# Optimization experiments

Hardware: AMD Instinct MI355X
Metric: run time of the kernel (lower is better)

The kernel has to match this reference:

```python
import jax, jax.numpy as jnp
import numpy as np
from jax import lax

B, C, H, W = 8, 128, 96, 96
EXPAN = 4           # expan_att_chans
NUM_CHANS = 2
NUM_HEADS = NUM_CHANS * EXPAN          # 8
HEAD_DIM = C * EXPAN // NUM_HEADS      # 64
EPS = 1e-12  # F.normalize eps


def _gconv(x, w, b, groups):
    # torch Conv2d(kernel=3, padding=1, groups=groups), OIHW weight layout
    y = lax.conv_general_dilated(x, w, (1, 1), 'SAME',
                                 feature_group_count=groups,
                                 dimension_numbers=('NCHW', 'OIHW', 'NCHW'))
    return y + b[None, :, None, None]


def setup_inputs() -> dict:
    key = jax.random.key(0)
    k0, k1, k2 = jax.random.split(key, 3)
    x = jax.random.normal(k0, (B, C, H, W), jnp.float32)
    w_qkv = jax.random.normal(k1, (C * EXPAN * 3, 1, 3, 3), jnp.float32) * 0.05
    b_qkv = jnp.zeros((C * EXPAN * 3,), jnp.float32)
    t = jnp.ones((1, NUM_HEADS, 1, 1), jnp.float32)
    w_fus = jax.random.normal(k2, (C, EXPAN, 3, 3), jnp.float32) * 0.05
    b_fus = jnp.zeros((C,), jnp.float32)
    return {"x": x, "w_qkv": w_qkv, "b_qkv": b_qkv, "t": t,
            "w_fus": w_fus, "b_fus": b_fus}


def reference(x, w_qkv, b_qkv, t, w_fus, b_fus):
    # depthwise-grouped qkv conv: [B, C*EXPAN*3, H, W]
    qkv = _gconv(x, w_qkv, b_qkv, C)
    # view(B, C, 3e, H, W).transpose(1,2) -> [B, 3e, C, H, W]
    qkv = qkv.reshape(B, C, 3 * EXPAN, H, W).transpose(0, 2, 1, 3, 4)
    q, k, v = jnp.split(qkv, 3, axis=1)  # each [B, EXPAN, C, H, W]

    def heads(a):
        return a.reshape(B, NUM_HEADS, HEAD_DIM, H * W)

    q, k, v = heads(q), heads(k), heads(v)

    def l2n(a):
        return a / jnp.maximum(jnp.linalg.norm(a, axis=-1, keepdims=True), EPS)

    q, k = l2n(q), l2n(k)
    attn = jnp.einsum('bhdn,bhen->bhde', q, k) * t   # [B, nh, hd, hd]
    attn = jax.nn.softmax(attn, axis=-1)
    o = jnp.einsum('bhde,bhen->bhdn', attn, v)       # [B, nh, hd, HW]
    # view(B, EXPAN, C, H, W).transpose(1,2).flatten(1,2) -> [B, C*EXPAN, H, W]
    o = o.reshape(B, EXPAN, C, H, W).transpose(0, 2, 1, 3, 4).reshape(B, C * EXPAN, H, W)
    return _gconv(o, w_fus, b_fus, C)
```

## Files before the change

kernel.cpp:

```cpp
#include <hip/hip_runtime.h>
#include <hip/hip_bf16.h>
#include <stdint.h>

#define BB     8
#define CC     128
#define HW     9216
#define NHEAD  8
#define HD     64
#define NCH    16
#define CHUNK  576

typedef __hip_bfloat16 bf16;
using frag16 = __attribute__((ext_vector_type(8))) short;
using f32x4  = __attribute__((ext_vector_type(4))) float;

__device__ __forceinline__ float b2f(bf16 v) { return __bfloat162float(v); }
__device__ __forceinline__ bf16  f2b(float v) { return __float2bfloat16(v); }

__device__ __forceinline__ float us2f(unsigned short u) {
  union { unsigned int i; float f; } c; c.i = ((unsigned int)u) << 16; return c.f;
}

__device__ __forceinline__ unsigned int pack2(float a, float b) {
  union { __hip_bfloat162 h2; unsigned int u; } c;
  c.h2 = __float22bfloat162_rn(make_float2(a, b));
  return c.u;
}

__global__ __launch_bounds__(256) void k1_qkv(
    const float* __restrict__ x, const float* __restrict__ wq,
    const float* __restrict__ bq,
    bf16* __restrict__ qg, bf16* __restrict__ kg, bf16* __restrict__ vg,
    float* __restrict__ qn2, float* __restrict__ kn2) {
  __shared__ float xs[98 * 100 + 4];
  __shared__ float red[32];
  int tid = threadIdx.x;
  int wave = tid >> 6, lane = tid & 63;
  int b = blockIdx.x >> 7, c = blockIdx.x & 127;
  const float* xp = x + (size_t)(b * CC + c) * HW;
  for (int i = tid; i < (98 * 100 + 4) / 4; i += 256)
    ((float4*)xs)[i] = make_float4(0.f, 0.f, 0.f, 0.f);
  __syncthreads();
  for (int i = tid; i < 96 * 24; i += 256) {
    int y = i / 24, g4 = i - y * 24;
    ((float4*)(xs + (y + 1) * 100 + 4))[g4] = ((const float4*)(xp + y * 96))[g4];
  }
  __syncthreads();

  int half = c >> 6, d = c & 63;
  int nidx[8];
  size_t basep[12];
#pragma unroll
  for (int j = 0; j < 12; ++j) {
    int e = j & 3;
    int h = e * 2 + half;
    int ni = (b * NHEAD + h) * HD + d;
    if (j < 8) nidx[j] = ni;
    basep[j] = (size_t)ni * HW;
  }
  const float* wrow = wq + c * 108;
  const float* brow = bq + c * 12;

  float ssq[8];
#pragma unroll
  for (int j = 0; j < 8; ++j) ssq[j] = 0.f;

#pragma unroll 1
  for (int it = 0; it < 9; ++it) {
    int q4i = it * 256 + tid;
    int y = q4i / 24;
    int xx = (q4i - y * 24) * 4;
    int p0 = y * 96 + xx;
    float w6[3][6];
#pragma unroll
    for (int ky = 0; ky < 3; ++ky) {
      int basea = (y + ky) * 100 + 4 + xx;
      float4 M = *(const float4*)&xs[basea];
      w6[ky][0] = xs[basea - 1];
      w6[ky][1] = M.x; w6[ky][2] = M.y; w6[ky][3] = M.z; w6[ky][4] = M.w;
      w6[ky][5] = xs[basea + 4];
    }
#pragma unroll
    for (int j = 0; j < 12; ++j) {
      float bias = brow[j];
      float a0 = bias, a1 = bias, a2 = bias, a3 = bias;
#pragma unroll
      for (int ky = 0; ky < 3; ++ky)
#pragma unroll
        for (int kx = 0; kx < 3; ++kx) {
          float w = wrow[j * 9 + ky * 3 + kx];
          a0 = fmaf(w, w6[ky][kx + 0], a0);
          a1 = fmaf(w, w6[ky][kx + 1], a1);
          a2 = fmaf(w, w6[ky][kx + 2], a2);
          a3 = fmaf(w, w6[ky][kx + 3], a3);
        }
      uint2 st = make_uint2(pack2(a0, a1), pack2(a2, a3));
      if (j < 4)      *(uint2*)(qg + basep[j] + p0) = st;
      else if (j < 8) *(uint2*)(kg + basep[j] + p0) = st;
      else            *(uint2*)(vg + basep[j] + p0) = st;
      if (j < 8)
        ssq[j] += a0 * a0 + a1 * a1 + a2 * a2 + a3 * a3;
    }
  }
#pragma unroll
  for (int j = 0; j < 8; ++j) {
    float v = ssq[j];
#pragma unroll
    for (int off = 32; off > 0; off >>= 1) v += __shfl_down(v, off);
    if (lane == 0) red[wave * 8 + j] = v;
  }
  __syncthreads();
  if (tid < 8) {
    float s = red[tid] + red[8 + tid] + red[16 + tid] + red[24 + tid];
    if (tid < 4) qn2[nidx[tid]] = s;
    else         kn2[nidx[tid]] = s;
  }
}

__global__ __launch_bounds__(256) void k2_gram(
    const bf16* __restrict__ qg, const bf16* __restrict__ kg,
    float* __restrict__ part) {
  int tid = threadIdx.x;
  int wave = tid >> 6;
  int lane = tid & 63;
  int chunk = blockIdx.x;
  int bh = blockIdx.y;
  const size_t base = (size_t)bh * HD * HW;
  int m = lane & 15;
  int k8 = (lane >> 4) * 8;
  const bf16* qrow  = qg + base + (size_t)(wave * 16 + m) * HW + k8;
  const bf16* krow0 = kg + base + (size_t)m * HW + k8;
  f32x4 acc0 = {0.f, 0.f, 0.f, 0.f}, acc1 = acc0, acc2 = acc0, acc3 = acc0;
  for (int kb = 0; kb < CHUNK; kb += 32) {
    int off = chunk * CHUNK + kb;
    frag16 a  = *(const frag16*)(qrow + off);
    frag16 b0 = *(const frag16*)(krow0 + off);
    frag16 b1 = *(const frag16*)(krow0 + (size_t)16 * HW + off);
    frag16 b2 = *(const frag16*)(krow0 + (size_t)32 * HW + off);
    frag16 b3 = *(const frag16*)(krow0 + (size_t)48 * HW + off);
    acc0 = __builtin_amdgcn_mfma_f32_16x16x32_bf16(a, b0, acc0, 0, 0, 0);
    acc1 = __builtin_amdgcn_mfma_f32_16x16x32_bf16(a, b1, acc1, 0, 0, 0);
    acc2 = __builtin_amdgcn_mfma_f32_16x16x32_bf16(a, b2, acc2, 0, 0, 0);
    acc3 = __builtin_amdgcn_mfma_f32_16x16x32_bf16(a, b3, acc3, 0, 0, 0);
  }
  float* po = part + (size_t)(bh * NCH + chunk) * 4096;
  int dr = wave * 16 + (lane >> 4) * 4;
  int e0 = lane & 15;
#pragma unroll
  for (int r = 0; r < 4; ++r) {
    po[(dr + r) * 64 +  0 + e0] = acc0[r];
    po[(dr + r) * 64 + 16 + e0] = acc1[r];
    po[(dr + r) * 64 + 32 + e0] = acc2[r];
    po[(dr + r) * 64 + 48 + e0] = acc3[r];
  }
}

__global__ __launch_bounds__(256) void k2_softmax(
    const float* __restrict__ part, bf16* __restrict__ ah, bf16* __restrict__ al,
    const float* __restrict__ qn2, const float* __restrict__ kn2,
    const float* __restrict__ t_f) {
  __shared__ float kns[64];
  int bh = blockIdx.x;
  int dq = blockIdx.y;
  int tid = threadIdx.x;
  if (tid < 64) kns[tid] = fmaxf(sqrtf(kn2[bh * 64 + tid]), 1e-12f);
  __syncthreads();
  int d  = dq * 16 + (tid >> 4);
  int e0 = (tid & 15) * 4;

  const float* pb = part + (size_t)bh * NCH * 4096 + d * 64 + e0;
  float4 s = make_float4(0.f, 0.f, 0.f, 0.f);
#pragma unroll
  for (int ch = 0; ch < NCH; ++ch) {
    float4 g = *(const float4*)&pb[ch * 4096];
    s.x += g.x; s.y += g.y; s.z += g.z; s.w += g.w;
  }
  float v[4] = {s.x, s.y, s.z, s.w};
  float sc = t_f[bh & 7] / fmaxf(sqrtf(qn2[bh * 64 + d]), 1e-12f);
  float m = -1e30f;
#pragma unroll
  for (int j = 0; j < 4; ++j) {
    v[j] = v[j] * sc / kns[e0 + j];
    m = fmaxf(m, v[j]);
  }
  m = fmaxf(m, __shfl_xor(m, 1));
  m = fmaxf(m, __shfl_xor(m, 2));
  m = fmaxf(m, __shfl_xor(m, 4));
  m = fmaxf(m, __shfl_xor(m, 8));
  float ssum = 0.f;
#pragma unroll
  for (int j = 0; j < 4; ++j) { v[j] = __expf(v[j] - m); ssum += v[j]; }
  ssum += __shfl_xor(ssum, 1);
  ssum += __shfl_xor(ssum, 2);
  ssum += __shfl_xor(ssum, 4);
  ssum += __shfl_xor(ssum, 8);
  float inv = 1.f / ssum;
  unsigned short hi16[4], lo16[4];
#pragma unroll
  for (int j = 0; j < 4; ++j) {
    float p = v[j] * inv;
    bf16 hi = f2b(p);
    float lo = p - b2f(hi);
    bf16 lov = f2b(lo);
    hi16[j] = *(unsigned short*)&hi;
    lo16[j] = *(unsigned short*)&lov;
  }
  const size_t base = (size_t)bh * 4096 + d * 64 + e0;
  *(ushort4*)(ah + base) = *(ushort4*)&hi16[0];
  *(ushort4*)(al + base) = *(ushort4*)&lo16[0];
}

__global__ __launch_bounds__(256) void k3_av(
    const bf16* __restrict__ ah, const bf16* __restrict__ al,
    const bf16* __restrict__ vg, bf16* __restrict__ og) {
  int tid = threadIdx.x;
  int wave = tid >> 6, lane = tid & 63;
  int chunk = blockIdx.x;
  int bh = blockIdx.y;
  int b = bh >> 3, h = bh & 7;
  int n0 = chunk * 256;
  int m = lane & 15;
  int k8 = (lane >> 4) * 8;
  int nwbase = wave * 64;

  const bf16* ahp = ah + (size_t)bh * 4096;
  const bf16* alp = al + (size_t)bh * 4096;
  frag16 a_hi[4][2], a_lo[4][2];
#pragma unroll
  for (int dt = 0; dt < 4; ++dt)
#pragma unroll
    for (int kh = 0; kh < 2; ++kh) {
      a_hi[dt][kh] = *(const frag16*)(ahp + (dt * 16 + m) * 64 + kh * 32 + k8);
      a_lo[dt][kh] = *(const frag16*)(alp + (dt * 16 + m) * 64 + kh * 32 + k8);
    }

  const bf16* vb = vg + (size_t)bh * HD * HW + n0 + nwbase + m;
  frag16 bfr[4][2];
#pragma unroll
  for (int kh = 0; kh < 2; ++kh)
#pragma unroll
    for (int j = 0; j < 8; ++j) {
      const bf16* vp = vb + (size_t)(kh * 32 + k8 + j) * HW;
      bfr[0][kh][j] = *(const short*)(vp);
      bfr[1][kh][j] = *(const short*)(vp + 16);
      bfr[2][kh][j] = *(const short*)(vp + 32);
      bfr[3][kh][j] = *(const short*)(vp + 48);
    }

  f32x4 acc[4][4];
#pragma unroll
  for (int dt = 0; dt < 4; ++dt)
#pragma unroll
    for (int nt = 0; nt < 4; ++nt) acc[dt][nt] = {0.f, 0.f, 0.f, 0.f};

#pragma unroll
  for (int nt = 0; nt < 4; ++nt)
#pragma unroll
    for (int kh = 0; kh < 2; ++kh)
#pragma unroll
      for (int dt = 0; dt < 4; ++dt) {
        acc[dt][nt] = __builtin_amdgcn_mfma_f32_16x16x32_bf16(a_hi[dt][kh], bfr[nt][kh], acc[dt][nt], 0, 0, 0);
        acc[dt][nt] = __builtin_amdgcn_mfma_f32_16x16x32_bf16(a_lo[dt][kh], bfr[nt][kh], acc[dt][nt], 0, 0, 0);
      }

  int cc0 = (h & 1) * 256 + (h >> 1);
  bf16* ob = og + (size_t)b * 512 * HW;
  int q4 = (lane >> 4) * 4;
#pragma unroll
  for (int dt = 0; dt < 4; ++dt)
#pragma unroll
    for (int nt = 0; nt < 4; ++nt) {
      int n = n0 + nwbase + nt * 16 + m;
#pragma unroll
      for (int r = 0; r < 4; ++r) {
        int d = dt * 16 + q4 + r;
        ob[(size_t)(cc0 + d * 4) * HW + n] = f2b(acc[dt][nt][r]);
      }
    }
}

__global__ __launch_bounds__(256) void k4_fuse(
    const bf16* __restrict__ og, const float* __restrict__ wf,
    const float* __restrict__ bfu, float* __restrict__ out) {
  __shared__ float lds[26 * 100 * 4];
  int tid = threadIdx.x;
  int tile = blockIdx.x;
  int bc = blockIdx.y;
  int b = bc >> 7, c = bc & 127;
  for (int i = tid; i < (26 * 100 * 4) / 4; i += 256)
    ((float4*)lds)[i] = make_float4(0.f, 0.f, 0.f, 0.f);
  __syncthreads();
  int r0 = tile * 24 - 1;
  const bf16* op = og + (size_t)(b * 512 + c * 4) * HW;
  for (int i = tid; i < 26 * 48; i += 256) {
    int rr = i / 48, xh = i - rr * 48;
    int gr = r0 + rr;
    if (gr >= 0 && gr < 96) {
      int gp = gr * 96 + xh * 2;
      ushort2 p0 = *(const ushort2*)(op + gp);
      ushort2 p1 = *(const ushort2*)(op + HW + gp);
      ushort2 p2 = *(const ushort2*)(op + 2 * HW + gp);
      ushort2 p3 = *(const ushort2*)(op + (size_t)3 * HW + gp);
      float* dst = &lds[(rr * 100 + 2 + xh * 2) * 4];
      *(float4*)dst       = make_float4(us2f(p0.x), us2f(p1.x), us2f(p2.x), us2f(p3.x));
      *(float4*)(dst + 4) = make_float4(us2f(p0.y), us2f(p1.y), us2f(p2.y), us2f(p3.y));
    }
  }
  __syncthreads();
  const float* wrow = wf + c * 36;
  float bias = bfu[c];
  float* outp = out + (size_t)(b * CC + c) * HW + tile * 24 * 96;
#pragma unroll
  for (int pi = 0; pi < 9; ++pi) {
    int p = pi * 256 + tid;
    int ry = p / 96, x = p - ry * 96;
    float a0 = bias, a1 = 0.f, a2 = 0.f, a3 = 0.f;
#pragma unroll
    for (int ky = 0; ky < 3; ++ky)
#pragma unroll
      for (int kx = 0; kx < 3; ++kx) {
        const float4 vv = *(const float4*)&lds[((ry + ky) * 100 + 1 + x + kx) * 4];
        a0 = fmaf(wrow[0 + ky * 3 + kx],  vv.x, a0);
        a1 = fmaf(wrow[9 + ky * 3 + kx],  vv.y, a1);
        a2 = fmaf(wrow[18 + ky * 3 + kx], vv.z, a2);
        a3 = fmaf(wrow[27 + ky * 3 + kx], vv.w, a3);
      }
    outp[p] = (a0 + a1) + (a2 + a3);
  }
}

extern "C" void kernel_launch(void* const* d_in, const int* in_sizes, int n_in,
                              void* d_out, int out_size, void* d_ws, size_t ws_size,
                              hipStream_t stream) {
  (void)in_sizes; (void)n_in; (void)out_size; (void)ws_size;
  const float* x   = (const float*)d_in[0];
  const float* wq  = (const float*)d_in[1];
  const float* bq  = (const float*)d_in[2];
  const float* tt  = (const float*)d_in[3];
  const float* wf  = (const float*)d_in[4];
  const float* bfu = (const float*)d_in[5];

  char* ws = (char*)d_ws;
  bf16*  qg    = (bf16*)(ws + 0);
  bf16*  kg    = (bf16*)(ws + 75497472);
  bf16*  vg    = (bf16*)(ws + 150994944);
  float* part  = (float*)(ws + 226492416);
  bf16*  ah    = (bf16*)(ws + 243269632);
  bf16*  al    = (bf16*)(ws + 243793920);
  float* qn2   = (float*)(ws + 244318208);
  float* kn2   = (float*)(ws + 244334592);
  bf16*  og    = qg;
  float* out   = (float*)d_out;

  hipLaunchKernelGGL(k1_qkv, dim3(1024), dim3(256), 0, stream,
                     x, wq, bq, qg, kg, vg, qn2, kn2);
  hipLaunchKernelGGL(k2_gram, dim3(NCH, 64), dim3(256), 0, stream, qg, kg, part);
  hipLaunchKernelGGL(k2_softmax, dim3(64, 4), dim3(256), 0, stream,
                     part, ah, al, qn2, kn2, tt);
  hipLaunchKernelGGL(k3_av, dim3(36, 64), dim3(256), 0, stream, ah, al, vg, og);
  hipLaunchKernelGGL(k4_fuse, dim3(4, 1024), dim3(256), 0, stream, og, wf, bfu, out);
}
```

Baseline: 260.1 us.

## Split qkv conv into row tiles, widen fuse loads, enlarge gram chunks

The depthwise qkv conv kernel now splits each (batch, channel) image into three 32-row tiles, giving three times as many blocks with smaller shared memory. Each tile writes its own partial squared norms, and the softmax kernel sums them. The gram kernel switches from 16 chunks of 576 to 12 chunks of 768, which cuts the partial buffer and the reduction work at the cost of fewer gram blocks. The fuse kernel loads bf16 data as 4-element vectors instead of 2-element ones. Together these aim to raise occupancy in the conv stage and cut memory-instruction overhead, at the cost of redundant halo-row loads.

After: 267.4 us. 1.03x slower.

```diff
diff --git a/kernel.cpp b/kernel.cpp
--- a/kernel.cpp
+++ b/kernel.cpp
@@ -7,8 +7,8 @@
 #define HW     9216
 #define NHEAD  8
 #define HD     64
-#define NCH    16
-#define CHUNK  576
+#define NCH    12
+#define CHUNK  768
 
 typedef __hip_bfloat16 bf16;
 using frag16 = __attribute__((ext_vector_type(8))) short;
@@ -31,19 +31,23 @@
     const float* __restrict__ x, const float* __restrict__ wq,
     const float* __restrict__ bq,
     bf16* __restrict__ qg, bf16* __restrict__ kg, bf16* __restrict__ vg,
-    float* __restrict__ qn2, float* __restrict__ kn2) {
-  __shared__ float xs[98 * 100 + 4];
+    float* __restrict__ qn2p, float* __restrict__ kn2p) {
+  __shared__ float xs[34 * 100 + 4];
   __shared__ float red[32];
   int tid = threadIdx.x;
   int wave = tid >> 6, lane = tid & 63;
   int b = blockIdx.x >> 7, c = blockIdx.x & 127;
+  int tile = blockIdx.y;
+  int r0 = tile * 32;
   const float* xp = x + (size_t)(b * CC + c) * HW;
-  for (int i = tid; i < (98 * 100 + 4) / 4; i += 256)
+  for (int i = tid; i < (34 * 100 + 4) / 4; i += 256)
     ((float4*)xs)[i] = make_float4(0.f, 0.f, 0.f, 0.f);
   __syncthreads();
-  for (int i = tid; i < 96 * 24; i += 256) {
-    int y = i / 24, g4 = i - y * 24;
-    ((float4*)(xs + (y + 1) * 100 + 4))[g4] = ((const float4*)(xp + y * 96))[g4];
+  for (int i = tid; i < 34 * 24; i += 256) {
+    int lr = i / 24, g4 = i - lr * 24;
+    int gr = r0 - 1 + lr;
+    if (gr >= 0 && gr < 96)
+      ((float4*)(xs + lr * 100 + 4))[g4] = ((const float4*)(xp + gr * 96))[g4];
   }
   __syncthreads();
 
@@ -66,15 +70,15 @@
   for (int j = 0; j < 8; ++j) ssq[j] = 0.f;
 
 #pragma unroll 1
-  for (int it = 0; it < 9; ++it) {
+  for (int it = 0; it < 3; ++it) {
     int q4i = it * 256 + tid;
-    int y = q4i / 24;
-    int xx = (q4i - y * 24) * 4;
-    int p0 = y * 96 + xx;
+    int ly = q4i / 24;
+    int xx = (q4i - ly * 24) * 4;
+    int p0 = (r0 + ly) * 96 + xx;
     float w6[3][6];
 #pragma unroll
     for (int ky = 0; ky < 3; ++ky) {
-      int basea = (y + ky) * 100 + 4 + xx;
+      int basea = (ly + ky) * 100 + 4 + xx;
       float4 M = *(const float4*)&xs[basea];
       w6[ky][0] = xs[basea - 1];
       w6[ky][1] = M.x; w6[ky][2] = M.y; w6[ky][3] = M.z; w6[ky][4] = M.w;
@@ -112,8 +116,8 @@
   __syncthreads();
   if (tid < 8) {
     float s = red[tid] + red[8 + tid] + red[16 + tid] + red[24 + tid];
-    if (tid < 4) qn2[nidx[tid]] = s;
-    else         kn2[nidx[tid]] = s;
+    if (tid < 4) qn2p[tile * 4096 + nidx[tid]] = s;
+    else         kn2p[tile * 4096 + nidx[tid]] = s;
   }
 }
 
@@ -157,13 +161,21 @@
 
 __global__ __launch_bounds__(256) void k2_softmax(
     const float* __restrict__ part, bf16* __restrict__ ah, bf16* __restrict__ al,
-    const float* __restrict__ qn2, const float* __restrict__ kn2,
+    const float* __restrict__ qn2p, const float* __restrict__ kn2p,
     const float* __restrict__ t_f) {
   __shared__ float kns[64];
+  __shared__ float qns[16];
   int bh = blockIdx.x;
   int dq = blockIdx.y;
   int tid = threadIdx.x;
-  if (tid < 64) kns[tid] = fmaxf(sqrtf(kn2[bh * 64 + tid]), 1e-12f);
+  if (tid < 64) {
+    float s = kn2p[bh * 64 + tid] + kn2p[4096 + bh * 64 + tid] + kn2p[8192 + bh * 64 + tid];
+    kns[tid] = fmaxf(sqrtf(s), 1e-12f);
+  } else if (tid < 80) {
+    int d = dq * 16 + (tid - 64);
+    float s = qn2p[bh * 64 + d] + qn2p[4096 + bh * 64 + d] + qn2p[8192 + bh * 64 + d];
+    qns[tid - 64] = fmaxf(sqrtf(s), 1e-12f);
+  }
   __syncthreads();
   int d  = dq * 16 + (tid >> 4);
   int e0 = (tid & 15) * 4;
@@ -176,7 +188,7 @@
     s.x += g.x; s.y += g.y; s.z += g.z; s.w += g.w;
   }
   float v[4] = {s.x, s.y, s.z, s.w};
-  float sc = t_f[bh & 7] / fmaxf(sqrtf(qn2[bh * 64 + d]), 1e-12f);
+  float sc = t_f[bh & 7] / qns[tid >> 4];
   float m = -1e30f;
 #pragma unroll
   for (int j = 0; j < 4; ++j) {
@@ -292,18 +304,20 @@
   __syncthreads();
   int r0 = tile * 24 - 1;
   const bf16* op = og + (size_t)(b * 512 + c * 4) * HW;
-  for (int i = tid; i < 26 * 48; i += 256) {
-    int rr = i / 48, xh = i - rr * 48;
+  for (int i = tid; i < 26 * 24; i += 256) {
+    int rr = i / 24, g4 = i - rr * 24;
     int gr = r0 + rr;
     if (gr >= 0 && gr < 96) {
-      int gp = gr * 96 + xh * 2;
-      ushort2 p0 = *(const ushort2*)(op + gp);
-      ushort2 p1 = *(const ushort2*)(op + HW + gp);
-      ushort2 p2 = *(const ushort2*)(op + 2 * HW + gp);
-      ushort2 p3 = *(const ushort2*)(op + (size_t)3 * HW + gp);
-      float* dst = &lds[(rr * 100 + 2 + xh * 2) * 4];
-      *(float4*)dst       = make_float4(us2f(p0.x), us2f(p1.x), us2f(p2.x), us2f(p3.x));
-      *(float4*)(dst + 4) = make_float4(us2f(p0.y), us2f(p1.y), us2f(p2.y), us2f(p3.y));
+      int gp = gr * 96 + g4 * 4;
+      ushort4 p0 = *(const ushort4*)(op + gp);
+      ushort4 p1 = *(const ushort4*)(op + HW + gp);
+      ushort4 p2 = *(const ushort4*)(op + 2 * HW + gp);
+      ushort4 p3 = *(const ushort4*)(op + (size_t)3 * HW + gp);
+      float* dst = &lds[(rr * 100 + 2 + g4 * 4) * 4];
+      *(float4*)(dst +  0) = make_float4(us2f(p0.x), us2f(p1.x), us2f(p2.x), us2f(p3.x));
+      *(float4*)(dst +  4) = make_float4(us2f(p0.y), us2f(p1.y), us2f(p2.y), us2f(p3.y));
+      *(float4*)(dst +  8) = make_float4(us2f(p0.z), us2f(p1.z), us2f(p2.z), us2f(p3.z));
+      *(float4*)(dst + 12) = make_float4(us2f(p0.w), us2f(p1.w), us2f(p2.w), us2f(p3.w));
     }
   }
   __syncthreads();
@@ -345,18 +359,18 @@
   bf16*  kg    = (bf16*)(ws + 75497472);
   bf16*  vg    = (bf16*)(ws + 150994944);
   float* part  = (float*)(ws + 226492416);
-  bf16*  ah    = (bf16*)(ws + 243269632);
-  bf16*  al    = (bf16*)(ws + 243793920);
-  float* qn2   = (float*)(ws + 244318208);
-  float* kn2   = (float*)(ws + 244334592);
+  bf16*  ah    = (bf16*)(ws + 239075328);
+  bf16*  al    = (bf16*)(ws + 239599616);
+  float* qn2p  = (float*)(ws + 240123904);
+  float* kn2p  = (float*)(ws + 240173056);
   bf16*  og    = qg;
   float* out   = (float*)d_out;
 
-  hipLaunchKernelGGL(k1_qkv, dim3(1024), dim3(256), 0, stream,
-                     x, wq, bq, qg, kg, vg, qn2, kn2);
+  hipLaunchKernelGGL(k1_qkv, dim3(1024, 3), dim3(256), 0, stream,
+                     x, wq, bq, qg, kg, vg, qn2p, kn2p);
   hipLaunchKernelGGL(k2_gram, dim3(NCH, 64), dim3(256), 0, stream, qg, kg, part);
   hipLaunchKernelGGL(k2_softmax, dim3(64, 4), dim3(256), 0, stream,
-                     part, ah, al, qn2, kn2, tt);
+                     part, ah, al, qn2p, kn2p, tt);
   hipLaunchKernelGGL(k3_av, dim3(36, 64), dim3(256), 0, stream, ah, al, vg, og);
   hipLaunchKernelGGL(k4_fuse, dim3(4, 1024), dim3(256), 0, stream, og, wf, bfu, out);
 }
```
